# Kernel optimization log

Measured on AMD Instinct MI355X. Metric: run time of the kernel, lower is better.

## Reference

```python
import jax, jax.numpy as jnp
import numpy as np

EPS = 1e-6


def setup_inputs() -> dict:
    key = jax.random.key(0)
    k1, k2 = jax.random.split(key)
    B, K, N, d = 4, 16, 2048, 256
    return {
        "img_f": jax.random.normal(k1, (B, K, d), dtype=jnp.float32),
        "text_f": jax.random.normal(k2, (N, K, d), dtype=jnp.float32),
        "r": jnp.zeros((4,), dtype=jnp.float32),
        "alp": jnp.array([0.5], dtype=jnp.float32),
        "scale": jnp.array([1.0], dtype=jnp.float32),
        "logits_scales": jnp.array([0.5], dtype=jnp.float32),
    }


def _rc_dist_ItoT(I, T, alpha, beta):
    # I: (B,K,d) images, T: (N,K,d) texts -> dist (B,N)
    B, K, d = I.shape
    lam = (B / d) * jnp.exp(alpha) + EPS
    rho = jnp.exp(beta)
    ItI = jnp.einsum('bkd,bke->bde', I, I)                      # (B,d,d)
    Minv = jnp.linalg.inv(ItI + lam * jnp.eye(d, dtype=I.dtype))
    A = jnp.einsum('bde,bke->bdk', Minv, I)                      # (B,d,K) = Minv @ I^T
    # T_bar[b,n] = I[b] @ A[b] @ T[n]; fuse P = I @ A (B,K,K) to avoid (B,N,d,d) W.
    P = jnp.einsum('bkd,bdj->bkj', I, A)                         # (B,K,K)
    T_bar = jnp.einsum('bkj,njd->bnkd', P, T) * rho              # (B,N,K,d)
    diff = T_bar - T[None]
    return -jnp.sum(diff * diff, axis=-1).mean(axis=-1)          # (B,N)


def _rc_dist_TtoI(I, T, alpha, beta):
    # per-text ridge projector applied to images -> dist (B,N)
    N, K, d = T.shape
    lam = (N / d) * jnp.exp(alpha) + EPS
    rho = jnp.exp(beta)
    TtT = jnp.einsum('nkd,nke->nde', T, T)                       # (N,d,d)
    Minv = jnp.linalg.inv(TtT + lam * jnp.eye(d, dtype=T.dtype))
    A = jnp.einsum('nde,nke->ndk', Minv, T)                      # (N,d,K)
    Q = jnp.einsum('nkd,ndj->nkj', T, A)                         # (N,K,K)
    I_bar = jnp.einsum('nkj,bjd->nbkd', Q, I) * rho              # (N,B,K,d)
    diff = I_bar - I[None]
    return (-jnp.sum(diff * diff, axis=-1).mean(axis=-1)).T      # (B,N)


def reference(img_f, text_f, r, alp, scale, logits_scales):
    d1 = _rc_dist_ItoT(img_f, text_f, r[0], r[1])
    d2 = _rc_dist_TtoI(img_f, text_f, r[2], r[3])
    rc_dist = alp * d1 + (1.0 - alp) * d2
    logits = rc_dist * scale
    logits_pre = jax.nn.log_softmax(logits, axis=1)
    return logits_pre, jax.nn.sigmoid(logits_scales)
```

## Files before the change

### kernel.cpp

```cpp
#include <hip/hip_runtime.h>
#include <math.h>

#define Bq 4
#define Kq 16
#define Nq 2048
#define Dq 256

typedef float f32x4 __attribute__((ext_vector_type(4)));
typedef short s16x8 __attribute__((ext_vector_type(8)));
typedef unsigned int u32;

union frag_u { s16x8 v; u32 w[4]; };

static __device__ __forceinline__ u32 cvtpk(float a, float b) {
    u32 r;
    asm("v_cvt_pk_bf16_f32 %0, %1, %2" : "=v"(r) : "v"(a), "v"(b));
    return r;
}

static __device__ __forceinline__ void cvt2(float a, float b, u32* hw, u32* lw) {
    const u32 h = cvtpk(a, b);
    const float h0 = __uint_as_float(h << 16);
    const float h1 = __uint_as_float(h & 0xFFFF0000u);
    *hw = h;
    *lw = cvtpk(a - h0, b - h1);
}

static __device__ __forceinline__ void conv8(const float4 a, const float4 b,
                                             s16x8* hi, s16x8* lo) {
    frag_u H, L;
    cvt2(a.x, a.y, &H.w[0], &L.w[0]);
    cvt2(a.z, a.w, &H.w[1], &L.w[1]);
    cvt2(b.x, b.y, &H.w[2], &L.w[2]);
    cvt2(b.z, b.w, &H.w[3], &L.w[3]);
    *hi = H.v; *lo = L.v;
}

#define MFMA(A, B, C) __builtin_amdgcn_mfma_f32_16x16x32_bf16((A), (B), (C), 0, 0, 0)

__global__ __launch_bounds__(256, 2) void fused_kernel(const float* __restrict__ img,
                                                       const float* __restrict__ text,
                                                       const float* __restrict__ r,
                                                       const float* __restrict__ alp,
                                                       const float* __restrict__ scale,
                                                       float* __restrict__ logits) {
    __shared__ __align__(16) float AugI[4][Kq][34];
    __shared__ __align__(16) float AugT[4][Kq][34];
    __shared__ __align__(16) f32x4 shS1[4][64];
    __shared__ __align__(16) f32x4 shGI[4][64];

    const int tid  = threadIdx.x;
    const int w    = tid >> 6, lane = tid & 63;
    const int arow = lane & 15, kgrp = lane >> 4, ccol = arow;
    const int n    = blockIdx.x * 4 + w;

    const float* baseI = img  + w * (Kq * Dq) + arow * Dq + kgrp * 8;
    const float* baseT = text + n * (Kq * Dq) + arow * Dq + kgrp * 8;
    float4 xi[16], xt[16];
#pragma unroll
    for (int c = 0; c < 8; ++c) {
        xi[2 * c]     = *reinterpret_cast<const float4*>(baseI + c * 32);
        xi[2 * c + 1] = *reinterpret_cast<const float4*>(baseI + c * 32 + 4);
    }
#pragma unroll
    for (int c = 0; c < 8; ++c) {
        xt[2 * c]     = *reinterpret_cast<const float4*>(baseT + c * 32);
        xt[2 * c + 1] = *reinterpret_cast<const float4*>(baseT + c * 32 + 4);
    }
    __builtin_amdgcn_sched_barrier(0);

    const float lamI = (float(Bq) / float(Dq)) * expf(r[0]) + 1e-6f;
    const float rhoI = expf(r[1]);
    const float lamT = (float(Nq) / float(Dq)) * expf(r[2]) + 1e-6f;
    const float rhoT = expf(r[3]);

    f32x4 gI = {0.f, 0.f, 0.f, 0.f};
#pragma unroll
    for (int c = 0; c < 8; ++c) {
        s16x8 hi, lo;
        conv8(xi[2 * c], xi[2 * c + 1], &hi, &lo);
        gI = MFMA(hi, hi, gI); gI = MFMA(hi, lo, gI); gI = MFMA(lo, hi, gI);
    }
    f32x4 gT = {0.f, 0.f, 0.f, 0.f};
#pragma unroll
    for (int c = 0; c < 8; ++c) {
        s16x8 hi, lo;
        conv8(xt[2 * c], xt[2 * c + 1], &hi, &lo);
        gT = MFMA(hi, hi, gT); gT = MFMA(hi, lo, gT); gT = MFMA(lo, hi, gT);
    }

    float (*AI)[34] = AugI[w];
    float (*AT)[34] = AugT[w];
#pragma unroll
    for (int q = 0; q < 4; ++q) {
        const int rr = kgrp * 4 + q;
        const float dI = (rr == ccol) ? lamI : 0.f;
        const float dT = (rr == ccol) ? lamT : 0.f;
        float2 pI; pI.x = gI[q] + dI; pI.y = (rhoI - 1.f) * gI[q] - dI;
        float2 pT; pT.x = gT[q] + dT; pT.y = (rhoT - 1.f) * gT[q] - dT;
        *reinterpret_cast<float2*>(&AI[rr][2 * ccol]) = pI;
        *reinterpret_cast<float2*>(&AT[rr][2 * ccol]) = pT;
    }
    __builtin_amdgcn_wave_barrier();

    for (int k = 0; k < Kq; ++k) {
        const float2 pvI = *reinterpret_cast<const float2*>(&AI[k][2 * k]);
        const float2 pvT = *reinterpret_cast<const float2*>(&AT[k][2 * k]);
        const float2 pkI = *reinterpret_cast<const float2*>(&AI[k][2 * ccol]);
        const float2 pkT = *reinterpret_cast<const float2*>(&AT[k][2 * ccol]);
        const float piI = 1.f / pvI.x;
        const float piT = 1.f / pvT.x;
        float facI[4], facT[4];
#pragma unroll
        for (int q = 0; q < 4; ++q) {
            facI[q] = AI[kgrp * 4 + q][2 * k];
            facT[q] = AT[kgrp * 4 + q][2 * k];
        }
        __builtin_amdgcn_wave_barrier();
#pragma unroll
        for (int q = 0; q < 4; ++q) {
            const int rr = kgrp * 4 + q;
            float2 cI = *reinterpret_cast<const float2*>(&AI[rr][2 * ccol]);
            float2 cT = *reinterpret_cast<const float2*>(&AT[rr][2 * ccol]);
            const float fI = facI[q] * piI;
            const float fT = facT[q] * piT;
            float2 nI, nT;
            nI.x = (rr == k) ? pkI.x * piI : cI.x - fI * pkI.x;
            nI.y = (rr == k) ? pkI.y * piI : cI.y - fI * pkI.y;
            nT.x = (rr == k) ? pkT.x * piT : cT.x - fT * pkT.x;
            nT.y = (rr == k) ? pkT.y * piT : cT.y - fT * pkT.y;
            *reinterpret_cast<float2*>(&AI[rr][2 * ccol]) = nI;
            *reinterpret_cast<float2*>(&AT[rr][2 * ccol]) = nT;
        }
        __builtin_amdgcn_wave_barrier();
    }

    frag_u HImg, LImg, HTxt, LTxt;
#pragma unroll
    for (int e = 0; e < 8; e += 2) {
        const int kk = (kgrp & 1) * 8 + e;
        const bool vld = (lane < 32);
        const float i0 = vld ? AI[arow][2 * kk + 1]       : 0.f;
        const float i1 = vld ? AI[arow][2 * (kk + 1) + 1] : 0.f;
        const float t0 = vld ? AT[arow][2 * kk + 1]       : 0.f;
        const float t1 = vld ? AT[arow][2 * (kk + 1) + 1] : 0.f;
        cvt2(i0, i1, &HImg.w[e >> 1], &LImg.w[e >> 1]);
        cvt2(t0, t1, &HTxt.w[e >> 1], &LTxt.w[e >> 1]);
    }
    f32x4 sI = {0.f, 0.f, 0.f, 0.f}, sT = {0.f, 0.f, 0.f, 0.f};
    sI = MFMA(HImg.v, HImg.v, sI); sI = MFMA(HImg.v, LImg.v, sI); sI = MFMA(LImg.v, HImg.v, sI);
    sT = MFMA(HTxt.v, HTxt.v, sT); sT = MFMA(HTxt.v, LTxt.v, sT); sT = MFMA(LTxt.v, HTxt.v, sT);

    shS1[w][lane] = sI;
    shGI[w][lane] = gI;
    __syncthreads();

    float p[8];
#pragma unroll
    for (int b = 0; b < 4; ++b) {
        const f32x4 s1 = shS1[b][lane];
        const f32x4 gi = shGI[b][lane];
        p[b]     = s1.x * gT.x + s1.y * gT.y + s1.z * gT.z + s1.w * gT.w;
        p[4 + b] = gi.x * sT.x + gi.y * sT.y + gi.z * sT.z + gi.w * sT.w;
    }
#pragma unroll
    for (int off = 32; off; off >>= 1) {
#pragma unroll
        for (int q = 0; q < 8; ++q) p[q] += __shfl_down(p[q], off, 64);
    }
    if (lane == 0) {
        const float a = alp[0], sc = scale[0];
#pragma unroll
        for (int b = 0; b < 4; ++b) {
            const float d1 = -p[b] * (1.f / Kq);
            const float d2 = -p[4 + b] * (1.f / Kq);
            logits[b * Nq + n] = sc * (a * d1 + (1.f - a) * d2);
        }
    }
}

__global__ __launch_bounds__(256) void softmax_kernel(const float* __restrict__ logits,
                                                      const float* __restrict__ lsc,
                                                      float* __restrict__ out) {
    const int b   = blockIdx.x;
    const int tid = threadIdx.x;
    const float* row = logits + b * Nq;
    __shared__ float sh[4];
    float v[8];
    float mx = -INFINITY;
#pragma unroll
    for (int q = 0; q < 8; ++q) {
        v[q] = row[tid + q * 256];
        mx = fmaxf(mx, v[q]);
    }
#pragma unroll
    for (int off = 32; off; off >>= 1) mx = fmaxf(mx, __shfl_down(mx, off, 64));
    if ((tid & 63) == 0) sh[tid >> 6] = mx;
    __syncthreads();
    mx = fmaxf(fmaxf(sh[0], sh[1]), fmaxf(sh[2], sh[3]));

    float sum = 0.f;
#pragma unroll
    for (int q = 0; q < 8; ++q) sum += expf(v[q] - mx);
#pragma unroll
    for (int off = 32; off; off >>= 1) sum += __shfl_down(sum, off, 64);
    __syncthreads();
    if ((tid & 63) == 0) sh[tid >> 6] = sum;
    __syncthreads();
    sum = sh[0] + sh[1] + sh[2] + sh[3];

    const float lse = mx + logf(sum);
#pragma unroll
    for (int q = 0; q < 8; ++q) out[b * Nq + tid + q * 256] = v[q] - lse;
    if (b == 0 && tid == 0) out[Bq * Nq] = 1.f / (1.f + expf(-lsc[0]));
}

extern "C" void kernel_launch(void* const* d_in, const int* in_sizes, int n_in,
                              void* d_out, int out_size, void* d_ws, size_t ws_size,
                              hipStream_t stream) {
    const float* img   = (const float*)d_in[0];
    const float* text  = (const float*)d_in[1];
    const float* r     = (const float*)d_in[2];
    const float* alp   = (const float*)d_in[3];
    const float* scale = (const float*)d_in[4];
    const float* lsc   = (const float*)d_in[5];
    float* ws  = (float*)d_ws;
    float* out = (float*)d_out;

    fused_kernel<<<Nq / 4, 256, 0, stream>>>(img, text, r, alp, scale, ws);
    softmax_kernel<<<Bq, 256, 0, stream>>>(ws, lsc, out);
}
```

Baseline: 24.32 us.

## Solve 16x16 ridge systems in registers with readlane Gauss-Jordan

The per-wave Gauss-Jordan elimination of the 16x16 augmented systems now runs in registers instead of shared memory. Lanes 0-15 handle the image system and lanes 16-31 the text system, with each lane owning one column, and pivots and row factors are broadcast through readlane. The loop over k is fully unrolled. This drops the repeated LDS reads and writes and the wave barriers inside the elimination, at the cost of many scalar readlane operations and higher register pressure. The result is written back to LDS once for the fragment conversion.

```diff
diff --git a/kernel.cpp b/kernel.cpp
--- a/kernel.cpp
+++ b/kernel.cpp
@@ -36,6 +36,10 @@
     *hi = H.v; *lo = L.v;
 }
 
+static __device__ __forceinline__ float rdlane(float x, int l) {
+    return __uint_as_float((u32)__builtin_amdgcn_readlane((int)__float_as_uint(x), l));
+}
+
 #define MFMA(A, B, C) __builtin_amdgcn_mfma_f32_16x16x32_bf16((A), (B), (C), 0, 0, 0)
 
 __global__ __launch_bounds__(256, 2) void fused_kernel(const float* __restrict__ img,
@@ -44,8 +48,7 @@
                                                        const float* __restrict__ alp,
                                                        const float* __restrict__ scale,
                                                        float* __restrict__ logits) {
-    __shared__ __align__(16) float AugI[4][Kq][34];
-    __shared__ __align__(16) float AugT[4][Kq][34];
+    __shared__ __align__(16) float scratch[4][2][16][20];
     __shared__ __align__(16) f32x4 shS1[4][64];
     __shared__ __align__(16) f32x4 shGI[4][64];
 
@@ -53,6 +56,8 @@
     const int w    = tid >> 6, lane = tid & 63;
     const int arow = lane & 15, kgrp = lane >> 4, ccol = arow;
     const int n    = blockIdx.x * 4 + w;
+    const bool isT = (lane & 16) != 0;
+    const int  sys = isT ? 1 : 0;
 
     const float* baseI = img  + w * (Kq * Dq) + arow * Dq + kgrp * 8;
     const float* baseT = text + n * (Kq * Dq) + arow * Dq + kgrp * 8;
@@ -89,61 +94,67 @@
         gT = MFMA(hi, hi, gT); gT = MFMA(hi, lo, gT); gT = MFMA(lo, hi, gT);
     }
 
-    float (*AI)[34] = AugI[w];
-    float (*AT)[34] = AugT[w];
-#pragma unroll
-    for (int q = 0; q < 4; ++q) {
-        const int rr = kgrp * 4 + q;
-        const float dI = (rr == ccol) ? lamI : 0.f;
-        const float dT = (rr == ccol) ? lamT : 0.f;
-        float2 pI; pI.x = gI[q] + dI; pI.y = (rhoI - 1.f) * gI[q] - dI;
-        float2 pT; pT.x = gT[q] + dT; pT.y = (rhoT - 1.f) * gT[q] - dT;
-        *reinterpret_cast<float2*>(&AI[rr][2 * ccol]) = pI;
-        *reinterpret_cast<float2*>(&AT[rr][2 * ccol]) = pT;
-    }
+    float (*Gc)[16][20] = scratch[w];
+    *reinterpret_cast<f32x4*>(&Gc[0][ccol][kgrp * 4]) = gI;
+    *reinterpret_cast<f32x4*>(&Gc[1][ccol][kgrp * 4]) = gT;
     __builtin_amdgcn_wave_barrier();
 
+    const int j = arow;
+    float A[16], rhs[16];
+    {
+        const float lam = isT ? lamT : lamI;
+        const float rho = isT ? rhoT : rhoI;
+        const float* col = &Gc[sys][j][0];
+        const f32x4 c0 = *reinterpret_cast<const f32x4*>(col + 0);
+        const f32x4 c1 = *reinterpret_cast<const f32x4*>(col + 4);
+        const f32x4 c2 = *reinterpret_cast<const f32x4*>(col + 8);
+        const f32x4 c3 = *reinterpret_cast<const f32x4*>(col + 12);
+        float g[16];
+#pragma unroll
+        for (int q = 0; q < 4; ++q) {
+            g[q] = c0[q]; g[4 + q] = c1[q]; g[8 + q] = c2[q]; g[12 + q] = c3[q];
+        }
+#pragma unroll
+        for (int i = 0; i < 16; ++i) {
+            const float dv = (i == j) ? lam : 0.f;
+            A[i]   = g[i] + dv;
+            rhs[i] = (rho - 1.f) * g[i] - dv;
+        }
+    }
+    __builtin_amdgcn_wave_barrier();
+
+#pragma unroll
     for (int k = 0; k < Kq; ++k) {
-        const float2 pvI = *reinterpret_cast<const float2*>(&AI[k][2 * k]);
-        const float2 pvT = *reinterpret_cast<const float2*>(&AT[k][2 * k]);
-        const float2 pkI = *reinterpret_cast<const float2*>(&AI[k][2 * ccol]);
-        const float2 pkT = *reinterpret_cast<const float2*>(&AT[k][2 * ccol]);
-        const float piI = 1.f / pvI.x;
-        const float piT = 1.f / pvT.x;
-        float facI[4], facT[4];
-#pragma unroll
-        for (int q = 0; q < 4; ++q) {
-            facI[q] = AI[kgrp * 4 + q][2 * k];
-            facT[q] = AT[kgrp * 4 + q][2 * k];
-        }
-        __builtin_amdgcn_wave_barrier();
-#pragma unroll
-        for (int q = 0; q < 4; ++q) {
-            const int rr = kgrp * 4 + q;
-            float2 cI = *reinterpret_cast<const float2*>(&AI[rr][2 * ccol]);
-            float2 cT = *reinterpret_cast<const float2*>(&AT[rr][2 * ccol]);
-            const float fI = facI[q] * piI;
-            const float fT = facT[q] * piT;
-            float2 nI, nT;
-            nI.x = (rr == k) ? pkI.x * piI : cI.x - fI * pkI.x;
-            nI.y = (rr == k) ? pkI.y * piI : cI.y - fI * pkI.y;
-            nT.x = (rr == k) ? pkT.x * piT : cT.x - fT * pkT.x;
-            nT.y = (rr == k) ? pkT.y * piT : cT.y - fT * pkT.y;
-            *reinterpret_cast<float2*>(&AI[rr][2 * ccol]) = nI;
-            *reinterpret_cast<float2*>(&AT[rr][2 * ccol]) = nT;
-        }
-        __builtin_amdgcn_wave_barrier();
-    }
+        const float pI = rdlane(A[k], k);
+        const float pT = rdlane(A[k], 16 + k);
+        const float pinv = 1.0f / (isT ? pT : pI);
+        A[k]   *= pinv;
+        rhs[k] *= pinv;
+#pragma unroll
+        for (int i = 0; i < 16; ++i) {
+            if (i == k) continue;
+            const float uI = rdlane(A[i], k);
+            const float uT = rdlane(A[i], 16 + k);
+            const float fac = isT ? uT : uI;
+            A[i]   = fmaf(-fac, A[k],   A[i]);
+            rhs[i] = fmaf(-fac, rhs[k], rhs[i]);
+        }
+    }
+
+    float (*Mr)[16][20] = scratch[w];
+#pragma unroll
+    for (int i = 0; i < 16; ++i) Mr[sys][i][j] = rhs[i];
+    __builtin_amdgcn_wave_barrier();
 
     frag_u HImg, LImg, HTxt, LTxt;
 #pragma unroll
     for (int e = 0; e < 8; e += 2) {
         const int kk = (kgrp & 1) * 8 + e;
         const bool vld = (lane < 32);
-        const float i0 = vld ? AI[arow][2 * kk + 1]       : 0.f;
-        const float i1 = vld ? AI[arow][2 * (kk + 1) + 1] : 0.f;
-        const float t0 = vld ? AT[arow][2 * kk + 1]       : 0.f;
-        const float t1 = vld ? AT[arow][2 * (kk + 1) + 1] : 0.f;
+        const float i0 = vld ? Mr[0][arow][kk]     : 0.f;
+        const float i1 = vld ? Mr[0][arow][kk + 1] : 0.f;
+        const float t0 = vld ? Mr[1][arow][kk]     : 0.f;
+        const float t1 = vld ? Mr[1][arow][kk + 1] : 0.f;
         cvt2(i0, i1, &HImg.w[e >> 1], &LImg.w[e >> 1]);
         cvt2(t0, t1, &HTxt.w[e >> 1], &LTxt.w[e >> 1]);
     }
```

Result: faster. 22.93 us (-5.7%).
